# Performance work log

Measured on AMD Instinct MI355X. Metric: run time of the kernel, lower is better.

Reference implementation:

```python
import jax, jax.numpy as jnp
import numpy as np

# --- static config (matches init_kwargs) ---
BATCH = 4
IN_CH = 32
OUT_CH = 32
H, W = 256, 256
CUTOFF = 0.02            # radius cutoff in normalized [0,1] coords
NR, NPHI = 6, 7          # kernel_shape: radial x angular basis counts
KSIZE = 1 + (NR - 1) * NPHI  # 36 basis functions (center + rings)
EPS = 1e-5               # InstanceNorm2d eps
SLOPE = 0.2              # LeakyReLU negative_slope


def _make_psi():
    """Fixed DISCO filter basis on the local equidistant patch.

    Returns [KSIZE, 2R+1, 2R+1]: piecewise-linear radial hats x periodic
    angular hats, supported inside the radius cutoff.
    """
    hy, hx = 1.0 / (H - 1), 1.0 / (W - 1)
    R = int(np.floor(CUTOFF * (min(H, W) - 1)))  # pixel radius (=5)
    iy, ix = np.meshgrid(np.arange(-R, R + 1), np.arange(-R, R + 1), indexing="ij")
    y, x = iy * hy, ix * hx
    r = np.sqrt(x * x + y * y)
    phi = np.mod(np.arctan2(y, x), 2.0 * np.pi)
    inside = (r <= CUTOFF).astype(np.float64)
    dr = CUTOFF / (NR - 1)
    dphi = 2.0 * np.pi / NPHI
    basis = [np.maximum(0.0, 1.0 - r / dr) * inside]  # isotropic center hat
    for j in range(1, NR):
        rad = np.maximum(0.0, 1.0 - np.abs(r - j * dr) / dr) * inside
        for k in range(NPHI):
            d = np.abs(np.mod(phi - k * dphi + np.pi, 2.0 * np.pi) - np.pi)
            ang = np.maximum(0.0, 1.0 - d / dphi)
            basis.append(rad * ang)
    return np.stack(basis).astype(np.float32)  # [36, 11, 11]


PSI = jnp.asarray(_make_psi())


def _disco_conv(x, w):
    # learned kernel = linear combination of fixed basis functions
    kern = jnp.einsum("oik,khw->oihw", w, PSI)  # [O, I, 11, 11]
    return jax.lax.conv_general_dilated(
        x, kern, window_strides=(1, 1), padding="SAME",
        dimension_numbers=("NCHW", "OIHW", "NCHW"))


def _instnorm_lrelu(x):
    # InstanceNorm2d (no affine) + LeakyReLU(0.2); Dropout2d is identity (eval)
    mu = jnp.mean(x, axis=(2, 3), keepdims=True)
    var = jnp.var(x, axis=(2, 3), keepdims=True)
    xn = (x - mu) * jax.lax.rsqrt(var + EPS)
    return jnp.where(xn >= 0, xn, SLOPE * xn)


def setup_inputs() -> dict:
    key = jax.random.key(0)
    k1, k2, k3 = jax.random.split(key, 3)
    image = jax.random.normal(k1, (BATCH, IN_CH, H, W), dtype=jnp.float32)
    scale = 1.0 / np.sqrt(IN_CH * KSIZE)
    weight1 = jax.random.normal(k2, (OUT_CH, IN_CH, KSIZE), dtype=jnp.float32) * scale
    weight2 = jax.random.normal(k3, (OUT_CH, OUT_CH, KSIZE), dtype=jnp.float32) * scale
    return {"image": image, "weight1": weight1, "weight2": weight2}


def reference(image, weight1, weight2):
    h = _instnorm_lrelu(_disco_conv(image, weight1))
    return _instnorm_lrelu(_disco_conv(h, weight2))
```

## Files before the change

kernel.cpp:

```cpp
#include <hip/hip_runtime.h>


typedef __attribute__((ext_vector_type(8))) short short8;
typedef __attribute__((ext_vector_type(4))) float f32x4;

#define NT      92
#define NSTEP   23
#define PSTR    27

__device__ inline ushort f2bf(float v) {
  uint u = __builtin_bit_cast(uint, v);
  return (ushort)((u + 0x7fffu + ((u >> 16) & 1u)) >> 16);
}
__device__ inline float bf2f(ushort h) {
  uint u = ((uint)h) << 16;
  return __builtin_bit_cast(float, u);
}

__global__ void build_kern_kernel(const float* __restrict__ w1,
                                  const float* __restrict__ w2,
                                  ushort* __restrict__ k1,
                                  ushort* __restrict__ k2) {
  __shared__ float psi[36 * 121];
  __shared__ int tpix[NT];
  const int blk   = blockIdx.x;
  const int layer = blk >> 5;
  const int i     = blk & 31;
  const int tid   = threadIdx.x;
  const double PI     = 3.141592653589793;
  const double TWO_PI = 6.283185307179586;
  for (int t = tid; t < 121; t += 128) {
    const int ky = t / 11, kx = t % 11;
    const double y = (ky - 5) / 255.0;
    const double x = (kx - 5) / 255.0;
    const double r = sqrt(x * x + y * y);
    double phi = atan2(y, x);
    if (phi < 0.0) phi += TWO_PI;
    const double inside = (r <= 0.02) ? 1.0 : 0.0;
    const double dr   = 0.02 / 5.0;
    const double dphi = TWO_PI / 7.0;
    psi[t] = (float)(fmax(0.0, 1.0 - r / dr) * inside);
    for (int j = 1; j < 6; ++j) {
      const double rad = fmax(0.0, 1.0 - fabs(r - j * dr) / dr) * inside;
      for (int k = 0; k < 7; ++k) {
        double d = fmod(phi - k * dphi + PI, TWO_PI);
        if (d < 0.0) d += TWO_PI;
        d = fabs(d - PI);
        const double ang = fmax(0.0, 1.0 - d / dphi);
        psi[(1 + (j - 1) * 7 + k) * 121 + t] = (float)(rad * ang);
      }
    }
  }
  if (tid == 0) {
    int c = 0;
    for (int kdy = 0; kdy < 11; ++kdy)
      for (int kdx = 0; kdx < 11; ++kdx)
        if ((kdy - 5) * (kdy - 5) + (kdx - 5) * (kdx - 5) <= 26)
          tpix[c++] = kdy * 11 + kdx;
    for (; c < NT; ++c) tpix[c] = -1;
  }
  __syncthreads();
  const float* w  = layer ? w2 : w1;
  ushort*      ko = layer ? k2 : k1;
  const int cch = i >> 3, j = i & 7;
  for (int idx = tid; idx < NT * 32; idx += 128) {
    const int t = idx >> 5;
    const int o = idx & 31;
    float s = 0.f;
    const int tp = tpix[t];
    if (tp >= 0) {
      const float* wp = w + (o * 32 + i) * 36;
#pragma unroll
      for (int k = 0; k < 36; ++k) s = fmaf(wp[k], psi[k * 121 + tp], s);
    }
    const ushort hi = f2bf(s);
    const ushort lo = f2bf(s - bf2f(hi));
    const int sk = t >> 2, q = t & 3, h = o >> 4;
    const int lane = (q << 4) | (o & 15);
    const size_t b0 = ((size_t)((cch * NSTEP + sk) * 2 + 0) * 2 + h) * 512 +
                      lane * 8 + j;
    const size_t b1 = ((size_t)((cch * NSTEP + sk) * 2 + 1) * 2 + h) * 512 +
                      lane * 8 + j;
    ko[b0] = hi;
    ko[b1] = lo;
  }
}

template <bool NORM_IN>
__global__ __launch_bounds__(256, 4)
void conv_mfma_kernel(const float* __restrict__ in,
                      const ushort* __restrict__ wpack,
                      float* __restrict__ out,
                      const float2* __restrict__ stats) {
  __shared__ __align__(16) ushort ph[26 * PSTR * 8];
  __shared__ __align__(16) ushort pl[26 * PSTR * 8];
  __shared__ int toffs[NT];
  const int tid = threadIdx.x;
  const int l   = tid & 63;
  const int wv  = tid >> 6;
  const int x   = l & 15;
  const int q   = l >> 4;
  const int bx0 = blockIdx.x * 16;
  const int by0 = blockIdx.y * 16;
  const int b   = blockIdx.z;

  if (tid == 0) {
    int c = 0;
    for (int kdy = 0; kdy < 11; ++kdy)
      for (int kdx = 0; kdx < 11; ++kdx)
        if ((kdy - 5) * (kdy - 5) + (kdx - 5) * (kdx - 5) <= 26)
          toffs[c++] = ((kdy - 5) * PSTR + (kdx - 5)) * 16;
    for (; c < NT; ++c) toffs[c] = 0;
  }

  f32x4 acc[2][4];
#pragma unroll
  for (int h = 0; h < 2; ++h)
#pragma unroll
    for (int g = 0; g < 4; ++g) {
      acc[h][g][0] = 0.f; acc[h][g][1] = 0.f;
      acc[h][g][2] = 0.f; acc[h][g][3] = 0.f;
    }

  int rowb[4];
#pragma unroll
  for (int g = 0; g < 4; ++g)
    rowb[g] = (((4 * wv + g + 5) * PSTR + 5) + x) * 16;

  for (int c = 0; c < 4; ++c) {
    __syncthreads();
    for (int idx = tid; idx < 8 * 26 * 26; idx += 256) {
      const int ci  = idx / 676;
      const int rem = idx - ci * 676;
      const int yy  = rem / 26;
      const int xx  = rem - yy * 26;
      const int gy  = by0 + yy - 5;
      const int gx  = bx0 + xx - 5;
      float v = 0.f;
      if ((unsigned)gy < 256u && (unsigned)gx < 256u) {
        v = in[(((b << 5) + (c << 3) + ci) << 16) + (gy << 8) + gx];
        if (NORM_IN) {
          const float2 st = stats[(b << 5) + (c << 3) + ci];
          v = (v - st.x) * st.y;
          v = v < 0.f ? 0.2f * v : v;
        }
      }
      const ushort hi = f2bf(v);
      const ushort lo = f2bf(v - bf2f(hi));
      ph[(yy * PSTR + xx) * 8 + ci] = hi;
      pl[(yy * PSTR + xx) * 8 + ci] = lo;
    }
    __syncthreads();
    const ushort* wc = wpack + (size_t)c * (NSTEP * 4 * 512);
    for (int s = 0; s < NSTEP; ++s) {
      const int toff = toffs[s * 4 + q];
      const ushort* wb = wc + s * 2048;
      const short8 Ah0 = *reinterpret_cast<const short8*>(wb + 0 * 512 + l * 8);
      const short8 Ah1 = *reinterpret_cast<const short8*>(wb + 1 * 512 + l * 8);
      const short8 Al0 = *reinterpret_cast<const short8*>(wb + 2 * 512 + l * 8);
      const short8 Al1 = *reinterpret_cast<const short8*>(wb + 3 * 512 + l * 8);
#pragma unroll
      for (int g = 0; g < 4; ++g) {
        const int off = rowb[g] + toff;
        const short8 Bh = *reinterpret_cast<const short8*>(
            reinterpret_cast<const char*>(ph) + off);
        const short8 Bl = *reinterpret_cast<const short8*>(
            reinterpret_cast<const char*>(pl) + off);
        acc[0][g] = __builtin_amdgcn_mfma_f32_16x16x32_bf16(Ah0, Bh, acc[0][g], 0, 0, 0);
        acc[1][g] = __builtin_amdgcn_mfma_f32_16x16x32_bf16(Ah1, Bh, acc[1][g], 0, 0, 0);
        acc[0][g] = __builtin_amdgcn_mfma_f32_16x16x32_bf16(Al0, Bh, acc[0][g], 0, 0, 0);
        acc[1][g] = __builtin_amdgcn_mfma_f32_16x16x32_bf16(Al1, Bh, acc[1][g], 0, 0, 0);
        acc[0][g] = __builtin_amdgcn_mfma_f32_16x16x32_bf16(Ah0, Bl, acc[0][g], 0, 0, 0);
        acc[1][g] = __builtin_amdgcn_mfma_f32_16x16x32_bf16(Ah1, Bl, acc[1][g], 0, 0, 0);
      }
    }
  }
  const int gx = bx0 + x;
#pragma unroll
  for (int h = 0; h < 2; ++h)
#pragma unroll
    for (int g = 0; g < 4; ++g) {
      const int gy = by0 + 4 * wv + g;
#pragma unroll
      for (int r = 0; r < 4; ++r) {
        const int oc = h * 16 + q * 4 + r;
        out[(((b << 5) + oc) << 16) + (gy << 8) + gx] = acc[h][g][r];
      }
    }
}

__global__ void stats_kernel(const float* __restrict__ y,
                             float2* __restrict__ stats) {
  const int bo  = blockIdx.x;
  const int tid = threadIdx.x;
  const float4* p = reinterpret_cast<const float4*>(y + (size_t)bo * 65536);
  float s = 0.f, q = 0.f;
  for (int i = tid; i < 16384; i += 256) {
    const float4 v = p[i];
    s += v.x + v.y + v.z + v.w;
    q += v.x * v.x + v.y * v.y + v.z * v.z + v.w * v.w;
  }
#pragma unroll
  for (int off = 32; off > 0; off >>= 1) {
    s += __shfl_down(s, off);
    q += __shfl_down(q, off);
  }
  __shared__ float sh[8];
  const int lane = tid & 63, wid = tid >> 6;
  if (lane == 0) { sh[wid] = s; sh[4 + wid] = q; }
  __syncthreads();
  if (tid == 0) {
    const float S = sh[0] + sh[1] + sh[2] + sh[3];
    const float Q = sh[4] + sh[5] + sh[6] + sh[7];
    const float mean = S * (1.f / 65536.f);
    const float var  = Q * (1.f / 65536.f) - mean * mean;
    stats[bo] = make_float2(mean, __frsqrt_rn(var + 1e-5f));
  }
}

__global__ void finalize_kernel(float* __restrict__ y,
                                const float2* __restrict__ stats) {
  const int n4 = (4 * 32 * 65536) / 4;
  float4* p = reinterpret_cast<float4*>(y);
  for (int i = blockIdx.x * blockDim.x + threadIdx.x; i < n4;
       i += gridDim.x * blockDim.x) {
    float4 v = p[i];
    const float2 st = stats[i >> 14];
    float t;
    t = (v.x - st.x) * st.y; v.x = t < 0.f ? 0.2f * t : t;
    t = (v.y - st.x) * st.y; v.y = t < 0.f ? 0.2f * t : t;
    t = (v.z - st.x) * st.y; v.z = t < 0.f ? 0.2f * t : t;
    t = (v.w - st.x) * st.y; v.w = t < 0.f ? 0.2f * t : t;
    p[i] = v;
  }
}

extern "C" void kernel_launch(void* const* d_in, const int* in_sizes, int n_in,
                              void* d_out, int out_size, void* d_ws,
                              size_t ws_size, hipStream_t stream) {
  const float* image = (const float*)d_in[0];
  const float* w1    = (const float*)d_in[1];
  const float* w2    = (const float*)d_in[2];
  float* out = (float*)d_out;
  float* ws  = (float*)d_ws;

  ushort* kern1  = (ushort*)ws;
  ushort* kern2  = (ushort*)(ws + 94208);
  float*  y1     = ws + 188416;
  float2* stats1 = (float2*)(ws + 188416 + 8388608);
  float2* stats2 = stats1 + 128;

  build_kern_kernel<<<64, 128, 0, stream>>>(w1, w2, kern1, kern2);

  dim3 cgrid(16, 16, 4);
  conv_mfma_kernel<false><<<cgrid, 256, 0, stream>>>(image, kern1, y1, nullptr);
  stats_kernel<<<128, 256, 0, stream>>>(y1, stats1);
  conv_mfma_kernel<true><<<cgrid, 256, 0, stream>>>(y1, kern2, out, stats1);
  stats_kernel<<<128, 256, 0, stream>>>(out, stats2);
  finalize_kernel<<<2048, 256, 0, stream>>>(out, stats2);
}
```

Before: 383.1 us.

## Fuse instance-norm statistics into conv epilogue, vectorize patch staging, prefetch weights

Measured after the change: 340.4 us. 11.2% less time.

```diff
diff --git a/kernel.cpp b/kernel.cpp
--- a/kernel.cpp
+++ b/kernel.cpp
@@ -86,15 +86,43 @@
   }
 }
 
+#define LOADW(W, S) do {                                                   \
+    const ushort* wb_ = wc + (size_t)(S) * 2048;                           \
+    W[0] = *reinterpret_cast<const short8*>(wb_ + 0 * 512 + l * 8);        \
+    W[1] = *reinterpret_cast<const short8*>(wb_ + 1 * 512 + l * 8);        \
+    W[2] = *reinterpret_cast<const short8*>(wb_ + 2 * 512 + l * 8);        \
+    W[3] = *reinterpret_cast<const short8*>(wb_ + 3 * 512 + l * 8);        \
+  } while (0)
+
+#define STEP(W, S) do {                                                    \
+    const int toff_ = toffs[(S) * 4 + q];                                  \
+    _Pragma("unroll")                                                      \
+    for (int g = 0; g < 4; ++g) {                                          \
+      const int off_ = rowb[g] + toff_;                                    \
+      const short8 Bh_ = *reinterpret_cast<const short8*>(                 \
+          reinterpret_cast<const char*>(ph) + off_);                       \
+      const short8 Bl_ = *reinterpret_cast<const short8*>(                 \
+          reinterpret_cast<const char*>(pl) + off_);                       \
+      acc[0][g] = __builtin_amdgcn_mfma_f32_16x16x32_bf16(W[0], Bh_, acc[0][g], 0, 0, 0); \
+      acc[1][g] = __builtin_amdgcn_mfma_f32_16x16x32_bf16(W[1], Bh_, acc[1][g], 0, 0, 0); \
+      acc[0][g] = __builtin_amdgcn_mfma_f32_16x16x32_bf16(W[2], Bh_, acc[0][g], 0, 0, 0); \
+      acc[1][g] = __builtin_amdgcn_mfma_f32_16x16x32_bf16(W[3], Bh_, acc[1][g], 0, 0, 0); \
+      acc[0][g] = __builtin_amdgcn_mfma_f32_16x16x32_bf16(W[0], Bl_, acc[0][g], 0, 0, 0); \
+      acc[1][g] = __builtin_amdgcn_mfma_f32_16x16x32_bf16(W[1], Bl_, acc[1][g], 0, 0, 0); \
+    }                                                                      \
+  } while (0)
+
 template <bool NORM_IN>
 __global__ __launch_bounds__(256, 4)
 void conv_mfma_kernel(const float* __restrict__ in,
                       const ushort* __restrict__ wpack,
                       float* __restrict__ out,
-                      const float2* __restrict__ stats) {
+                      const float2* __restrict__ stats,
+                      float* __restrict__ accum) {
   __shared__ __align__(16) ushort ph[26 * PSTR * 8];
   __shared__ __align__(16) ushort pl[26 * PSTR * 8];
   __shared__ int toffs[NT];
+  __shared__ float2 psum[4][32];
   const int tid = threadIdx.x;
   const int l   = tid & 63;
   const int wv  = tid >> 6;
@@ -129,51 +157,45 @@
 
   for (int c = 0; c < 4; ++c) {
     __syncthreads();
-    for (int idx = tid; idx < 8 * 26 * 26; idx += 256) {
-      const int ci  = idx / 676;
-      const int rem = idx - ci * 676;
-      const int yy  = rem / 26;
-      const int xx  = rem - yy * 26;
-      const int gy  = by0 + yy - 5;
-      const int gx  = bx0 + xx - 5;
-      float v = 0.f;
+    for (int idx = tid; idx < 26 * 26; idx += 256) {
+      const int yy = idx / 26;
+      const int xx = idx - yy * 26;
+      const int gy = by0 + yy - 5;
+      const int gx = bx0 + xx - 5;
+      short8 h8 = {0, 0, 0, 0, 0, 0, 0, 0};
+      short8 l8 = {0, 0, 0, 0, 0, 0, 0, 0};
       if ((unsigned)gy < 256u && (unsigned)gx < 256u) {
-        v = in[(((b << 5) + (c << 3) + ci) << 16) + (gy << 8) + gx];
-        if (NORM_IN) {
-          const float2 st = stats[(b << 5) + (c << 3) + ci];
-          v = (v - st.x) * st.y;
-          v = v < 0.f ? 0.2f * v : v;
+        const float* ip = in + (((b << 5) + (c << 3)) << 16) + (gy << 8) + gx;
+#pragma unroll
+        for (int ci = 0; ci < 8; ++ci) {
+          float v = ip[ci << 16];
+          if (NORM_IN) {
+            const float2 st = stats[(b << 5) + (c << 3) + ci];
+            v = (v - st.x) * st.y;
+            v = v < 0.f ? 0.2f * v : v;
+          }
+          const ushort hi = f2bf(v);
+          const ushort lo = f2bf(v - bf2f(hi));
+          h8[ci] = (short)hi;
+          l8[ci] = (short)lo;
         }
       }
-      const ushort hi = f2bf(v);
-      const ushort lo = f2bf(v - bf2f(hi));
-      ph[(yy * PSTR + xx) * 8 + ci] = hi;
-      pl[(yy * PSTR + xx) * 8 + ci] = lo;
+      const int lidx = (yy * PSTR + xx) * 8;
+      *reinterpret_cast<short8*>(&ph[lidx]) = h8;
+      *reinterpret_cast<short8*>(&pl[lidx]) = l8;
     }
     __syncthreads();
     const ushort* wc = wpack + (size_t)c * (NSTEP * 4 * 512);
-    for (int s = 0; s < NSTEP; ++s) {
-      const int toff = toffs[s * 4 + q];
-      const ushort* wb = wc + s * 2048;
-      const short8 Ah0 = *reinterpret_cast<const short8*>(wb + 0 * 512 + l * 8);
-      const short8 Ah1 = *reinterpret_cast<const short8*>(wb + 1 * 512 + l * 8);
-      const short8 Al0 = *reinterpret_cast<const short8*>(wb + 2 * 512 + l * 8);
-      const short8 Al1 = *reinterpret_cast<const short8*>(wb + 3 * 512 + l * 8);
-#pragma unroll
-      for (int g = 0; g < 4; ++g) {
-        const int off = rowb[g] + toff;
-        const short8 Bh = *reinterpret_cast<const short8*>(
-            reinterpret_cast<const char*>(ph) + off);
-        const short8 Bl = *reinterpret_cast<const short8*>(
-            reinterpret_cast<const char*>(pl) + off);
-        acc[0][g] = __builtin_amdgcn_mfma_f32_16x16x32_bf16(Ah0, Bh, acc[0][g], 0, 0, 0);
-        acc[1][g] = __builtin_amdgcn_mfma_f32_16x16x32_bf16(Ah1, Bh, acc[1][g], 0, 0, 0);
-        acc[0][g] = __builtin_amdgcn_mfma_f32_16x16x32_bf16(Al0, Bh, acc[0][g], 0, 0, 0);
-        acc[1][g] = __builtin_amdgcn_mfma_f32_16x16x32_bf16(Al1, Bh, acc[1][g], 0, 0, 0);
-        acc[0][g] = __builtin_amdgcn_mfma_f32_16x16x32_bf16(Ah0, Bl, acc[0][g], 0, 0, 0);
-        acc[1][g] = __builtin_amdgcn_mfma_f32_16x16x32_bf16(Ah1, Bl, acc[1][g], 0, 0, 0);
-      }
-    }
+    short8 Wa[4], Wb[4];
+    LOADW(Wa, 0);
+    int s = 0;
+    for (; s + 1 < NSTEP; s += 2) {
+      LOADW(Wb, s + 1);
+      STEP(Wa, s);
+      if (s + 2 < NSTEP) LOADW(Wa, s + 2);
+      STEP(Wb, s + 1);
+    }
+    STEP(Wa, NSTEP - 1);
   }
   const int gx = bx0 + x;
 #pragma unroll
@@ -187,33 +209,42 @@
         out[(((b << 5) + oc) << 16) + (gy << 8) + gx] = acc[h][g][r];
       }
     }
-}
-
-__global__ void stats_kernel(const float* __restrict__ y,
-                             float2* __restrict__ stats) {
-  const int bo  = blockIdx.x;
-  const int tid = threadIdx.x;
-  const float4* p = reinterpret_cast<const float4*>(y + (size_t)bo * 65536);
-  float s = 0.f, q = 0.f;
-  for (int i = tid; i < 16384; i += 256) {
-    const float4 v = p[i];
-    s += v.x + v.y + v.z + v.w;
-    q += v.x * v.x + v.y * v.y + v.z * v.z + v.w * v.w;
-  }
-#pragma unroll
-  for (int off = 32; off > 0; off >>= 1) {
-    s += __shfl_down(s, off);
-    q += __shfl_down(q, off);
-  }
-  __shared__ float sh[8];
-  const int lane = tid & 63, wid = tid >> 6;
-  if (lane == 0) { sh[wid] = s; sh[4 + wid] = q; }
+#pragma unroll
+  for (int h = 0; h < 2; ++h)
+#pragma unroll
+    for (int r = 0; r < 4; ++r) {
+      float s = 0.f, qq = 0.f;
+#pragma unroll
+      for (int g = 0; g < 4; ++g) {
+        const float v = acc[h][g][r];
+        s += v; qq += v * v;
+      }
+#pragma unroll
+      for (int m = 1; m < 16; m <<= 1) {
+        s  += __shfl_xor(s, m, 64);
+        qq += __shfl_xor(qq, m, 64);
+      }
+      if (x == 0) psum[wv][h * 16 + q * 4 + r] = make_float2(s, qq);
+    }
   __syncthreads();
-  if (tid == 0) {
-    const float S = sh[0] + sh[1] + sh[2] + sh[3];
-    const float Q = sh[4] + sh[5] + sh[6] + sh[7];
-    const float mean = S * (1.f / 65536.f);
-    const float var  = Q * (1.f / 65536.f) - mean * mean;
+  if (tid < 32) {
+    const float2 a0 = psum[0][tid], a1 = psum[1][tid];
+    const float2 a2 = psum[2][tid], a3 = psum[3][tid];
+    atomicAdd(&accum[(b * 32 + tid) * 2 + 0], a0.x + a1.x + a2.x + a3.x);
+    atomicAdd(&accum[(b * 32 + tid) * 2 + 1], a0.y + a1.y + a2.y + a3.y);
+  }
+}
+
+__global__ void zero_kernel(float* __restrict__ accum) {
+  if (threadIdx.x < 512) accum[threadIdx.x] = 0.f;
+}
+
+__global__ void statsfix_kernel(const float* __restrict__ accum,
+                                float2* __restrict__ stats) {
+  const int bo = threadIdx.x;
+  if (bo < 128) {
+    const float mean = accum[bo * 2 + 0] * (1.f / 65536.f);
+    const float var  = accum[bo * 2 + 1] * (1.f / 65536.f) - mean * mean;
     stats[bo] = make_float2(mean, __frsqrt_rn(var + 1e-5f));
   }
 }
@@ -247,15 +278,20 @@
   ushort* kern1  = (ushort*)ws;
   ushort* kern2  = (ushort*)(ws + 94208);
   float*  y1     = ws + 188416;
-  float2* stats1 = (float2*)(ws + 188416 + 8388608);
+  float*  accum1 = ws + 188416 + 8388608;
+  float*  accum2 = accum1 + 256;
+  float2* stats1 = (float2*)(accum1 + 512);
   float2* stats2 = stats1 + 128;
 
   build_kern_kernel<<<64, 128, 0, stream>>>(w1, w2, kern1, kern2);
+  zero_kernel<<<1, 512, 0, stream>>>(accum1);
 
   dim3 cgrid(16, 16, 4);
-  conv_mfma_kernel<false><<<cgrid, 256, 0, stream>>>(image, kern1, y1, nullptr);
-  stats_kernel<<<128, 256, 0, stream>>>(y1, stats1);
-  conv_mfma_kernel<true><<<cgrid, 256, 0, stream>>>(y1, kern2, out, stats1);
-  stats_kernel<<<128, 256, 0, stream>>>(out, stats2);
+  conv_mfma_kernel<false><<<cgrid, 256, 0, stream>>>(image, kern1, y1,
+                                                     nullptr, accum1);
+  statsfix_kernel<<<1, 128, 0, stream>>>(accum1, stats1);
+  conv_mfma_kernel<true><<<cgrid, 256, 0, stream>>>(y1, kern2, out,
+                                                    stats1, accum2);
+  statsfix_kernel<<<1, 128, 0, stream>>>(accum2, stats2);
   finalize_kernel<<<2048, 256, 0, stream>>>(out, stats2);
 }
```
